# Optimization experiments

Measured on AMD Instinct MI355X. Metric: run time of the kernel, lower is better.

The kernel has to match this reference:

```python
import jax, jax.numpy as jnp
import numpy as np

NUM_EMBEDDINGS = 1024
EMBEDDING_DIM = 256
COMMITMENT_COST = 0.25


def setup_inputs() -> dict:
    key = jax.random.key(0)
    k1, k2 = jax.random.split(key)
    x = jax.random.normal(k1, (32, EMBEDDING_DIM, 32, 32), dtype=jnp.float32)
    codebook = jax.random.uniform(
        k2, (NUM_EMBEDDINGS, EMBEDDING_DIM), dtype=jnp.float32,
        minval=-1.0 / NUM_EMBEDDINGS, maxval=1.0 / NUM_EMBEDDINGS)
    return {"x": x, "codebook": codebook}


def reference(x, codebook):
    # x: [B, C, H, W] -> [B, H, W, C]
    inputs = jnp.transpose(x, (0, 2, 3, 1))
    B, H, W, D = inputs.shape
    K = codebook.shape[0]
    flat = inputs.reshape(-1, D)  # [N, D]

    # squared L2 distances to each code: [N, K]
    distances = (jnp.sum(flat ** 2, axis=1, keepdims=True)
                 + jnp.sum(codebook ** 2, axis=1)
                 - 2.0 * flat @ codebook.T)
    idx = jnp.argmin(distances, axis=1)  # [N]

    # gather codes (equivalent to one-hot @ codebook, without materializing one-hot)
    quantized = codebook[idx].reshape(inputs.shape)

    e_latent_loss = jnp.mean((jax.lax.stop_gradient(quantized) - inputs) ** 2)
    q_latent_loss = jnp.mean((quantized - jax.lax.stop_gradient(inputs)) ** 2)
    loss = q_latent_loss + COMMITMENT_COST * e_latent_loss

    # straight-through estimator
    quantized_st = inputs + jax.lax.stop_gradient(quantized - inputs)

    # perplexity from code usage histogram (mean of one-hot encodings)
    N = flat.shape[0]
    avg_probs = jnp.zeros((K,), dtype=flat.dtype).at[idx].add(1.0) / N
    perplexity = jnp.exp(-jnp.sum(avg_probs * jnp.log(avg_probs + 1e-10)))

    out = jnp.transpose(quantized_st, (0, 3, 1, 2))  # back to [B, C, H, W]
    return (out, loss, perplexity)
```

## Files before the change

kernel.cpp:

```cpp
#include <hip/hip_runtime.h>
#include <hip/hip_fp16.h>

typedef _Float16 half8 __attribute__((ext_vector_type(8)));
typedef _Float16 half4v __attribute__((ext_vector_type(4)));
typedef __attribute__((ext_vector_type(4))) float f32x4;

#define OUT_ELEMS 8388608


__global__ __launch_bounds__(256) void prep_kernel(const float* __restrict__ cb,
        unsigned short* __restrict__ chs, float* __restrict__ sq,
        int* __restrict__ counts, float* __restrict__ loss) {
    const int t = threadIdx.x;
    if (blockIdx.x == 0) {
        ((int4*)counts)[t] = make_int4(0, 0, 0, 0);
        if (t == 0) *loss = 0.f;
    }
    const int row = blockIdx.x * 16 + (t >> 4);
    const int d0 = (t & 15) * 16;
    const float* src = cb + row * 256 + d0;
    half8 h0, h1;
    float s = 0.f;
#pragma unroll
    for (int i = 0; i < 16; ++i) {
        const float v = src[i];
        s += v * v;
        const _Float16 h = (_Float16)(v * 1024.f);
        if (i < 8) h0[i] = h; else h1[i - 8] = h;
    }
    *(half8*)(chs + row * 256 + d0)     = h0;
    *(half8*)(chs + row * 256 + d0 + 8) = h1;
#pragma unroll
    for (int off = 1; off < 16; off <<= 1) s += __shfl_xor(s, off);
    if ((t & 15) == 0) sq[row] = s;
}

__global__ __launch_bounds__(512, 2) void vq_kernel(
    const float* __restrict__ x, const float* __restrict__ cb,
    const unsigned short* __restrict__ chs, const float* __restrict__ sq,
    int* __restrict__ counts, float* __restrict__ loss_accum,
    float* __restrict__ out)
{
    __shared__ __align__(16) unsigned char Arena[65536];
    __shared__ float mv[4][128];
    __shared__ int   mk[4][128];
    __shared__ float xsqL[128];
    __shared__ int   codeL[128];
    __shared__ float wsum[2];

    const int t = threadIdx.x;
    const int lane = t & 63;
    const int w  = t >> 6;
    const int wg = w >> 1;
    const int wl = w & 1;
    const int m = lane & 15;
    const int q = lane >> 4;
    const int kb = wg << 8;
    const int rowb = wl << 6;
    const int bid = blockIdx.x;
    const int batch = bid >> 3;
    const int hwb = (bid & 7) << 7;

    const int cs = t >> 3, sg = cs >> 4, sm = cs & 15;
    const int sj0 = (t & 7) * 4;
    const unsigned short* srow = chs + ((sg << 8) + sm) * 256 + sj0 * 8;
    half8 n0, n1, n2, n3;
    n0 = *(const half8*)(srow);
    n1 = *(const half8*)(srow + 8);
    n2 = *(const half8*)(srow + 16);
    n3 = *(const half8*)(srow + 24);
    float sc2 = sq[kb + m];

    unsigned short* XL = (unsigned short*)Arena;
    {
        const float* xg = x + (size_t)batch * 262144 + hwb;
#pragma unroll
        for (int p = 0; p < 4; ++p) {
            const int id = p * 512 + t;
            const int c4 = id >> 5;
            const int hw4 = id & 31;
            const float* s0 = xg + (size_t)(c4 * 4) * 1024 + hw4 * 4;
            const f32x4 v0 = *(const f32x4*)(s0);
            const f32x4 v1 = *(const f32x4*)(s0 + 1024);
            const f32x4 v2 = *(const f32x4*)(s0 + 2048);
            const f32x4 v3 = *(const f32x4*)(s0 + 3072);
#pragma unroll
            for (int j = 0; j < 4; ++j) {
                const int hw = hw4 * 4 + j;
                const int e = (((hw & 7) ^ ((hw >> 3) & 7)) << 1);
                half4v hv;
                hv[0] = (_Float16)v0[j];
                hv[1] = (_Float16)v1[j];
                hv[2] = (_Float16)v2[j];
                hv[3] = (_Float16)v3[j];
                *(half4v*)(XL + hw * 256 + ((c4 ^ e) << 2)) = hv;
            }
        }
    }
    __syncthreads();

    half8 Ah[4][8];
#pragma unroll
    for (int f = 0; f < 4; ++f) {
        const int hw = rowb + f * 16 + m;
        const unsigned short* row = XL + hw * 256;
        const int e = (((hw & 7) ^ ((hw >> 3) & 7)) << 1);
        float xs = 0.f;
#pragma unroll
        for (int ks = 0; ks < 8; ++ks) {
            const half8 a = *(const half8*)(row + (((8 * ks + 2 * q) ^ e) << 2));
            Ah[f][ks] = a;
#pragma unroll
            for (int j = 0; j < 8; ++j) { const float fv = (float)a[j]; xs = fmaf(fv, fv, xs); }
        }
        xs += __shfl_xor(xs, 16);
        xs += __shfl_xor(xs, 32);
        if (wg == 0 && q == 0) xsqL[hw] = xs;
    }
    __syncthreads();

    unsigned short* Bs = (unsigned short*)Arena;
    {
        unsigned short* wb = Bs + cs * 256;
        *(half8*)(wb + (((sj0 + 0) ^ (sm & 7)) << 3)) = n0;
        *(half8*)(wb + (((sj0 + 1) ^ (sm & 7)) << 3)) = n1;
        *(half8*)(wb + (((sj0 + 2) ^ (sm & 7)) << 3)) = n2;
        *(half8*)(wb + (((sj0 + 3) ^ (sm & 7)) << 3)) = n3;
    }

    float bestv[4][4];
    int   bestk[4][4];
#pragma unroll
    for (int f = 0; f < 4; ++f)
#pragma unroll
        for (int r = 0; r < 4; ++r) { bestv[f][r] = 3.4e38f; bestk[f][r] = 0; }

    const unsigned short* brow = Bs + (wg * 16 + m) * 256;
    const int eswz = m & 7;

    for (int s = 0; s < 16; ++s) {
        const int buf = s & 1;
        float sqn = 0.f;
        if (s + 1 < 16) {
            const unsigned short* sp = srow + (s + 1) * 4096;
            n0 = *(const half8*)(sp);
            n1 = *(const half8*)(sp + 8);
            n2 = *(const half8*)(sp + 16);
            n3 = *(const half8*)(sp + 24);
            sqn = sq[kb + (s + 1) * 16 + m];
        }
        __syncthreads();
        f32x4 a0 = {0.f,0.f,0.f,0.f}, a1 = {0.f,0.f,0.f,0.f};
        f32x4 a2 = {0.f,0.f,0.f,0.f}, a3 = {0.f,0.f,0.f,0.f};
        const unsigned short* bp = brow + buf * 16384;
#pragma unroll
        for (int ks = 0; ks < 8; ++ks) {
            const half8 b = *(const half8*)(bp + (((ks * 4 + q) ^ eswz) << 3));
            a0 = __builtin_amdgcn_mfma_f32_16x16x32_f16(Ah[0][ks], b, a0, 0, 0, 0);
            a1 = __builtin_amdgcn_mfma_f32_16x16x32_f16(Ah[1][ks], b, a1, 0, 0, 0);
            a2 = __builtin_amdgcn_mfma_f32_16x16x32_f16(Ah[2][ks], b, a2, 0, 0, 0);
            a3 = __builtin_amdgcn_mfma_f32_16x16x32_f16(Ah[3][ks], b, a3, 0, 0, 0);
        }
        const int code = kb + s * 16 + m;
#pragma unroll
        for (int f = 0; f < 4; ++f) {
            const f32x4 a = (f == 0) ? a0 : (f == 1) ? a1 : (f == 2) ? a2 : a3;
#pragma unroll
            for (int r = 0; r < 4; ++r) {
                const float d0v = fmaf(-0.001953125f, a[r], sc2);
                if (d0v < bestv[f][r]) { bestv[f][r] = d0v; bestk[f][r] = code; }
            }
        }
        if (s + 1 < 16) {
            unsigned short* wb = Bs + (buf ^ 1) * 16384 + cs * 256;
            *(half8*)(wb + (((sj0 + 0) ^ (sm & 7)) << 3)) = n0;
            *(half8*)(wb + (((sj0 + 1) ^ (sm & 7)) << 3)) = n1;
            *(half8*)(wb + (((sj0 + 2) ^ (sm & 7)) << 3)) = n2;
            *(half8*)(wb + (((sj0 + 3) ^ (sm & 7)) << 3)) = n3;
            sc2 = sqn;
        }
    }

#pragma unroll
    for (int f = 0; f < 4; ++f)
#pragma unroll
        for (int r = 0; r < 4; ++r) {
            float v = bestv[f][r];
            int   k = bestk[f][r];
#pragma unroll
            for (int d = 1; d < 16; d <<= 1) {
                const float ov = __shfl_xor(v, d);
                const int   ok = __shfl_xor(k, d);
                if (ov < v || (ov == v && ok < k)) { v = ov; k = ok; }
            }
            if (m == 0) {
                const int row = rowb + f * 16 + q * 4 + r;
                mv[wg][row] = v;
                mk[wg][row] = k;
            }
        }
    __syncthreads();

    if (t < 128) {
        float v = mv[0][t]; int k = mk[0][t];
#pragma unroll
        for (int g2 = 1; g2 < 4; ++g2) {
            const float vg = mv[g2][t];
            const int   kg = mk[g2][t];
            if (vg < v) { v = vg; k = kg; }
        }
        codeL[t] = k;
        atomicAdd(&counts[k], 1);
        float lp = xsqL[t] + v;
#pragma unroll
        for (int off = 32; off > 0; off >>= 1) lp += __shfl_down(lp, off);
        if ((t & 63) == 0) wsum[t >> 6] = lp;
    }
    __syncthreads();
    if (t == 0) atomicAdd(loss_accum, wsum[0] + wsum[1]);

    float* Q = (float*)Arena;
#pragma unroll
    for (int h = 0; h < 4; ++h) {
        {
            const int r = t & 31, seg = t >> 5;
            const float* src = cb + (size_t)codeL[h * 32 + r] * 256 + seg * 16;
#pragma unroll
            for (int i = 0; i < 4; ++i)
                *(f32x4*)&Q[r * 257 + seg * 16 + i * 4] = *(const f32x4*)(src + i * 4);
        }
        __syncthreads();
        {
            const int hw4 = (t & 7) * 4;
            const int c0 = t >> 3;
            float* dst = out + (size_t)batch * 262144 + hwb + h * 32 + hw4;
#pragma unroll
            for (int i = 0; i < 4; ++i) {
                const int c = c0 + i * 64;
                f32x4 v;
                v[0] = Q[(hw4 + 0) * 257 + c];
                v[1] = Q[(hw4 + 1) * 257 + c];
                v[2] = Q[(hw4 + 2) * 257 + c];
                v[3] = Q[(hw4 + 3) * 257 + c];
                *(f32x4*)(dst + (size_t)c * 1024) = v;
            }
        }
        if (h < 3) __syncthreads();
    }
}

__global__ __launch_bounds__(256) void finalize_kernel(
    const int* __restrict__ counts, const float* __restrict__ loss_accum,
    float* __restrict__ out)
{
    __shared__ float wsum[4];
    const int t = threadIdx.x;
    float s = 0.f;
#pragma unroll
    for (int mm = 0; mm < 4; ++mm) {
        const float p = (float)counts[t + 256 * mm] * (1.f / 32768.f);
        s += p * logf(p + 1e-10f);
    }
#pragma unroll
    for (int off = 32; off > 0; off >>= 1) s += __shfl_down(s, off);
    if ((t & 63) == 0) wsum[t >> 6] = s;
    __syncthreads();
    if (t == 0) {
        out[OUT_ELEMS]     = loss_accum[0] * (1.25f / 8388608.f);
        out[OUT_ELEMS + 1] = expf(-(wsum[0] + wsum[1] + wsum[2] + wsum[3]));
    }
}

extern "C" void kernel_launch(void* const* d_in, const int* in_sizes, int n_in,
                              void* d_out, int out_size, void* d_ws, size_t ws_size,
                              hipStream_t stream) {
    const float* x  = (const float*)d_in[0];
    const float* cb = (const float*)d_in[1];
    float* out = (float*)d_out;
    char* wsb = (char*)d_ws;
    int*            counts = (int*)(wsb + 0);
    float*          loss   = (float*)(wsb + 4096);
    float*          sq     = (float*)(wsb + 8192);
    unsigned short* chs    = (unsigned short*)(wsb + 16384);

    prep_kernel<<<64, 256, 0, stream>>>(cb, chs, sq, counts, loss);
    vq_kernel<<<256, 512, 0, stream>>>(x, cb, chs, sq, counts, loss, out);
    finalize_kernel<<<1, 256, 0, stream>>>(counts, loss, out);
}
```

Baseline: 124.8 us.

## Load codebook MFMA operands directly from global memory instead of LDS staging

Removes the double-buffered LDS staging of the fp16 codebook tile and the per-step block barrier. Each wave now loads its B fragments straight from global memory (L2-resident codebook) into registers before the MFMA loop. This avoids the LDS writes, reads and __syncthreads in the inner loop, but each wave pair now loads the same codebook rows separately and there is no software prefetch to hide global latency.

```diff
diff --git a/kernel.cpp b/kernel.cpp
--- a/kernel.cpp
+++ b/kernel.cpp
@@ -61,16 +61,6 @@
     const int batch = bid >> 3;
     const int hwb = (bid & 7) << 7;
 
-    const int cs = t >> 3, sg = cs >> 4, sm = cs & 15;
-    const int sj0 = (t & 7) * 4;
-    const unsigned short* srow = chs + ((sg << 8) + sm) * 256 + sj0 * 8;
-    half8 n0, n1, n2, n3;
-    n0 = *(const half8*)(srow);
-    n1 = *(const half8*)(srow + 8);
-    n2 = *(const half8*)(srow + 16);
-    n3 = *(const half8*)(srow + 24);
-    float sc2 = sq[kb + m];
-
     unsigned short* XL = (unsigned short*)Arena;
     {
         const float* xg = x + (size_t)batch * 262144 + hwb;
@@ -117,16 +107,6 @@
         xs += __shfl_xor(xs, 32);
         if (wg == 0 && q == 0) xsqL[hw] = xs;
     }
-    __syncthreads();
-
-    unsigned short* Bs = (unsigned short*)Arena;
-    {
-        unsigned short* wb = Bs + cs * 256;
-        *(half8*)(wb + (((sj0 + 0) ^ (sm & 7)) << 3)) = n0;
-        *(half8*)(wb + (((sj0 + 1) ^ (sm & 7)) << 3)) = n1;
-        *(half8*)(wb + (((sj0 + 2) ^ (sm & 7)) << 3)) = n2;
-        *(half8*)(wb + (((sj0 + 3) ^ (sm & 7)) << 3)) = n3;
-    }
 
     float bestv[4][4];
     int   bestk[4][4];
@@ -135,31 +115,26 @@
 #pragma unroll
         for (int r = 0; r < 4; ++r) { bestv[f][r] = 3.4e38f; bestk[f][r] = 0; }
 
-    const unsigned short* brow = Bs + (wg * 16 + m) * 256;
-    const int eswz = m & 7;
+    float sc2 = sq[kb + m];
+
+    const unsigned short* bgl = chs + (size_t)(kb + m) * 256 + q * 8;
 
     for (int s = 0; s < 16; ++s) {
-        const int buf = s & 1;
         float sqn = 0.f;
-        if (s + 1 < 16) {
-            const unsigned short* sp = srow + (s + 1) * 4096;
-            n0 = *(const half8*)(sp);
-            n1 = *(const half8*)(sp + 8);
-            n2 = *(const half8*)(sp + 16);
-            n3 = *(const half8*)(sp + 24);
-            sqn = sq[kb + (s + 1) * 16 + m];
-        }
-        __syncthreads();
+        if (s + 1 < 16) sqn = sq[kb + (s + 1) * 16 + m];
+        half8 Bf[8];
+        const unsigned short* bp = bgl + s * 4096;
+#pragma unroll
+        for (int ks = 0; ks < 8; ++ks)
+            Bf[ks] = *(const half8*)(bp + ks * 32);
         f32x4 a0 = {0.f,0.f,0.f,0.f}, a1 = {0.f,0.f,0.f,0.f};
         f32x4 a2 = {0.f,0.f,0.f,0.f}, a3 = {0.f,0.f,0.f,0.f};
-        const unsigned short* bp = brow + buf * 16384;
 #pragma unroll
         for (int ks = 0; ks < 8; ++ks) {
-            const half8 b = *(const half8*)(bp + (((ks * 4 + q) ^ eswz) << 3));
-            a0 = __builtin_amdgcn_mfma_f32_16x16x32_f16(Ah[0][ks], b, a0, 0, 0, 0);
-            a1 = __builtin_amdgcn_mfma_f32_16x16x32_f16(Ah[1][ks], b, a1, 0, 0, 0);
-            a2 = __builtin_amdgcn_mfma_f32_16x16x32_f16(Ah[2][ks], b, a2, 0, 0, 0);
-            a3 = __builtin_amdgcn_mfma_f32_16x16x32_f16(Ah[3][ks], b, a3, 0, 0, 0);
+            a0 = __builtin_amdgcn_mfma_f32_16x16x32_f16(Ah[0][ks], Bf[ks], a0, 0, 0, 0);
+            a1 = __builtin_amdgcn_mfma_f32_16x16x32_f16(Ah[1][ks], Bf[ks], a1, 0, 0, 0);
+            a2 = __builtin_amdgcn_mfma_f32_16x16x32_f16(Ah[2][ks], Bf[ks], a2, 0, 0, 0);
+            a3 = __builtin_amdgcn_mfma_f32_16x16x32_f16(Ah[3][ks], Bf[ks], a3, 0, 0, 0);
         }
         const int code = kb + s * 16 + m;
 #pragma unroll
@@ -171,14 +146,7 @@
                 if (d0v < bestv[f][r]) { bestv[f][r] = d0v; bestk[f][r] = code; }
             }
         }
-        if (s + 1 < 16) {
-            unsigned short* wb = Bs + (buf ^ 1) * 16384 + cs * 256;
-            *(half8*)(wb + (((sj0 + 0) ^ (sm & 7)) << 3)) = n0;
-            *(half8*)(wb + (((sj0 + 1) ^ (sm & 7)) << 3)) = n1;
-            *(half8*)(wb + (((sj0 + 2) ^ (sm & 7)) << 3)) = n2;
-            *(half8*)(wb + (((sj0 + 3) ^ (sm & 7)) << 3)) = n3;
-            sc2 = sqn;
-        }
+        sc2 = sqn;
     }
 
 #pragma unroll
```

New measurement: 134.7 us. 8.0% more time.
